# Kernel tuning notes

Measured on AMD Instinct MI355X. Metric: run time of the kernel, lower is better.

Reference implementation:

```python
import jax, jax.numpy as jnp
import numpy as np

NEG_INF = -jnp.inf


def setup_inputs() -> dict:
    B, V = 128, 128000
    key = jax.random.key(0)
    k1, k2, k3, k4, k5 = jax.random.split(key, 5)
    logits = jax.random.normal(k1, (B, V), dtype=jnp.float32)
    # temperatures in [0.1, 1.0) to avoid divide-by-tiny blowups
    temperatures = jax.random.uniform(k2, (B,), dtype=jnp.float32) * 0.9 + 0.1
    # min_p typically small, in [0, 0.1)
    min_ps = jax.random.uniform(k3, (B,), dtype=jnp.float32) * 0.1
    # top_p in [0.1, 1.0)
    top_ps = jax.random.uniform(k4, (B,), dtype=jnp.float32) * 0.9 + 0.1
    # top_k in [1, 1000)
    top_ks = jax.random.randint(k5, (B,), 1, 1000, dtype=jnp.int32)
    return {"logits": logits, "temperatures": temperatures, "min_ps": min_ps,
            "top_ps": top_ps, "top_ks": top_ks}


def _apply_top_k_top_p(logits, top_ps, top_ks):
    B, V = logits.shape
    sort_idx = jnp.argsort(logits, axis=-1)  # ascending, matches torch sort(descending=False)
    logits_sort = jnp.take_along_axis(logits, sort_idx, axis=-1)
    # top-k: threshold is the (V-k)-th smallest value; mask anything strictly below it
    thresh_idx = (V - top_ks.astype(jnp.int32))[:, None]          # [B,1]
    thresh = jnp.take_along_axis(logits_sort, thresh_idx, axis=-1)  # [B,1]
    logits_sort = jnp.where(logits_sort < thresh, NEG_INF, logits_sort)
    # top-p: drop smallest tokens whose cumulative prob <= 1 - p; never drop the max token
    probs_sort = jax.nn.softmax(logits_sort, axis=-1)
    probs_sum = jnp.cumsum(probs_sort, axis=-1)
    top_p_mask = probs_sum <= (1.0 - top_ps)[:, None]
    top_p_mask = top_p_mask.at[:, -1].set(False)
    logits_sort = jnp.where(top_p_mask, NEG_INF, logits_sort)
    # scatter back to original vocab order
    rows = jnp.arange(B)[:, None]
    return jnp.zeros_like(logits_sort).at[rows, sort_idx].set(logits_sort)


def _apply_min_p(logits, min_ps):
    probs = jax.nn.softmax(logits, axis=-1)
    top_probs = jnp.max(probs, axis=-1, keepdims=True)
    remove = probs < min_ps[:, None] * top_probs
    return jnp.where(remove, NEG_INF, logits)


def reference(logits, temperatures, min_ps, top_ps, top_ks):
    logits = logits.astype(jnp.float32) / temperatures[:, None]
    logits = _apply_top_k_top_p(logits, top_ps, top_ks)
    logits = _apply_min_p(logits, min_ps)
    # torch.multinomial(softmax(logits), 1) == categorical sampling from logits
    sample_key = jax.random.key(42)
    next_tokens = jax.random.categorical(sample_key, logits, axis=-1)  # [B]
    return next_tokens
```

## Files before the change

kernel.cpp:

```cpp
#include <hip/hip_runtime.h>
#include <stdint.h>

#define HBINS 8192
#define HSHIFT 19
#define CAND 2048
#define STHREADS 1024

typedef unsigned int u32;
typedef unsigned long long u64;

__device__ __forceinline__ u32 f2s(float f) {
  u32 b = __float_as_uint(f);
  return b ^ ((b & 0x80000000u) ? 0xFFFFFFFFu : 0x80000000u);
}
__device__ __forceinline__ float s2f(u32 s) {
  u32 b = (s & 0x80000000u) ? (s ^ 0x80000000u) : ~s;
  return __uint_as_float(b);
}
__device__ __forceinline__ u32 rotl32(u32 x, int r) { return (x << r) | (x >> (32 - r)); }

__device__ __forceinline__ u64 shfl_xor_u64(u64 v, int mask) {
  int lo = __shfl_xor((int)(u32)v, mask, 64);
  int hi = __shfl_xor((int)(u32)(v >> 32), mask, 64);
  return ((u64)(u32)hi << 32) | (u32)lo;
}
__device__ __forceinline__ u64 shfl_down_u64(u64 v, int delta) {
  int lo = __shfl_down((int)(u32)v, delta, 64);
  int hi = __shfl_down((int)(u32)(v >> 32), delta, 64);
  return ((u64)(u32)hi << 32) | (u32)lo;
}

__device__ __forceinline__ u32 threefry_bits(u32 ctr) {
  const u32 ks0 = 0u, ks1 = 42u, ks2 = 0x1BD11BDAu ^ 0u ^ 42u;
  u32 x0 = ks0;
  u32 x1 = ctr + ks1;
#define TFR(r) { x0 += x1; x1 = rotl32(x1, (r)); x1 ^= x0; }
  TFR(13) TFR(15) TFR(26) TFR(6)   x0 += ks1; x1 += ks2 + 1u;
  TFR(17) TFR(29) TFR(16) TFR(24)  x0 += ks2; x1 += ks0 + 2u;
  TFR(13) TFR(15) TFR(26) TFR(6)   x0 += ks0; x1 += ks1 + 3u;
  TFR(17) TFR(29) TFR(16) TFR(24)  x0 += ks1; x1 += ks2 + 4u;
  TFR(13) TFR(15) TFR(26) TFR(6)   x0 += ks2; x1 += ks0 + 5u;
#undef TFR
  return x0 ^ x1;
}

__global__ __launch_bounds__(STHREADS)
void Sampler_73529840107542_kernel(const float* __restrict__ logits,
                                   const float* __restrict__ temps,
                                   const float* __restrict__ minps,
                                   const float* __restrict__ topps,
                                   const int* __restrict__ topks,
                                   int* __restrict__ out, int V) {
  const int row = blockIdx.x;
  const int tid = threadIdx.x;
  const int w = tid >> 6;
  const int l = tid & 63;

  __shared__ __align__(16) unsigned char arena[69632];
  u32* hp     = (u32*)arena;
  u32* part   = (u32*)(arena + 65536);
  u64* cand   = (u64*)arena;
  u64* cand2  = (u64*)(arena + 16384);
  float* bufA = (float*)(arena + 16384);
  float* bufB = (float*)(arena + 24576);
  unsigned char* keepf = arena + 32768;
  float* redA = (float*)(arena + 16384);
  float* redB = (float*)(arena + 24576);

  __shared__ int sh_pstar, sh_cnt, sh_lb, sh_cs;
  __shared__ u32 sh_thr, sh_Ts;
  __shared__ float sh_m, sh_Z1, sh_Z2;
  __shared__ u32 wsum[16], wsuf[16];
  __shared__ u64 wbest[16];

  for (int i = tid; i < 2 * HBINS; i += STHREADS) hp[i] = 0u;
  __syncthreads();
  const float* src = logits + (size_t)row * (size_t)V;
  const u32 pc = (u32)(tid & 1);
  const int n4 = V >> 2;
  const float4* p4 = (const float4*)src;
  const int BB = STHREADS * 8;
  for (int base_i = 0; base_i < n4; base_i += BB) {
    float4 v[8];
    bool ok[8];
#pragma unroll
    for (int j = 0; j < 8; ++j) {
      int i = base_i + j * STHREADS + tid;
      ok[j] = (i < n4);
      v[j] = ok[j] ? p4[i] : float4{0.f, 0.f, 0.f, 0.f};
    }
#pragma unroll
    for (int j = 0; j < 8; ++j) {
      if (ok[j]) {
        atomicAdd(&hp[((f2s(v[j].x) >> HSHIFT) << 1) | pc], 1u);
        atomicAdd(&hp[((f2s(v[j].y) >> HSHIFT) << 1) | pc], 1u);
        atomicAdd(&hp[((f2s(v[j].z) >> HSHIFT) << 1) | pc], 1u);
        atomicAdd(&hp[((f2s(v[j].w) >> HSHIFT) << 1) | pc], 1u);
      }
    }
  }
  for (int i = (n4 << 2) + tid; i < V; i += STHREADS)
    atomicAdd(&hp[((f2s(src[i]) >> HSHIFT) << 1) | pc], 1u);
  __syncthreads();

  u32 pv;
  {
    u32 s = 0;
#pragma unroll
    for (int j = 0; j < 16; ++j) s += hp[tid * 16 + j];
    pv = s;
  }
#pragma unroll
  for (int d = 1; d < 64; d <<= 1) {
    u32 o = (u32)__shfl_down((int)pv, d, 64);
    if (l + d < 64) pv += o;
  }
  if (l == 0) wsum[w] = pv;
  __syncthreads();
  if (w == 0) {
    u32 v = (l < 16) ? wsum[l] : 0u;
#pragma unroll
    for (int d = 1; d < 64; d <<= 1) {
      u32 o = (u32)__shfl_down((int)v, d, 64);
      if (l + d < 64) v += o;
    }
    if (l < 16) wsuf[l] = v;
  }
  __syncthreads();
  part[tid] = pv + ((w < 15) ? wsuf[w + 1] : 0u);
  __syncthreads();

  int k = topks[row];
  if (k < 1) k = 1;
  if (k > V) k = V;
  const u32 ku = (u32)k;
  if (part[tid] >= ku && (tid == STHREADS - 1 || part[tid + 1] < ku))
    sh_pstar = tid;
  __syncthreads();
  {
    const int pstar = sh_pstar;
    const u32 tail = (pstar < STHREADS - 1) ? part[pstar + 1] : 0u;
    if (tid < 8) {
      u32 sb = tail;
      for (int j = 7; j >= tid; --j) sb += hp[(pstar * 8 + j) * 2] + hp[(pstar * 8 + j) * 2 + 1];
      u32 own = hp[(pstar * 8 + tid) * 2] + hp[(pstar * 8 + tid) * 2 + 1];
      if (sb >= ku && (tid == 7 || sb - own < ku)) {
        sh_thr = (u32)(pstar * 8 + tid) << HSHIFT;
        sh_cs = (int)((sb < (u32)CAND) ? sb : (u32)CAND);
      }
    }
    if (tid == 0) sh_cnt = 0;
  }
  __syncthreads();

  const u32 thr = sh_thr;
  const float t = temps[row];
  for (int base_i = 0; base_i < n4; base_i += BB) {
    float4 v[8];
    bool ok[8];
#pragma unroll
    for (int j = 0; j < 8; ++j) {
      int i = base_i + j * STHREADS + tid;
      ok[j] = (i < n4);
      v[j] = ok[j] ? p4[i] : float4{0.f, 0.f, 0.f, 0.f};
    }
#pragma unroll
    for (int j = 0; j < 8; ++j) {
      const int i = base_i + j * STHREADS + tid;
      float vals[4] = {v[j].x, v[j].y, v[j].z, v[j].w};
#pragma unroll
      for (int cmp = 0; cmp < 4; ++cmp) {
        bool pred = ok[j] && (f2s(vals[cmp]) >= thr);
        u64 mk = __ballot(pred);
        if (mk) {
          int leader = __ffsll((long long)mk) - 1;
          int tot = __popcll(mk);
          int b0 = 0;
          if (l == leader) b0 = atomicAdd(&sh_cnt, tot);
          b0 = __shfl(b0, leader, 64);
          if (pred) {
            int pos = b0 + __popcll(mk & ((1ull << l) - 1ull));
            if (pos < CAND)
              cand[pos] = ((u64)f2s(vals[cmp] / t) << 32) | (u32)(4 * i + cmp);
          }
        }
      }
    }
  }
  for (int i = (n4 << 2) + tid; i < V; i += STHREADS) {
    float x = src[i];
    if (f2s(x) >= thr) { int pos = atomicAdd(&sh_cnt, 1); if (pos < CAND) cand[pos] = ((u64)f2s(x / t) << 32) | (u32)i; }
  }
  __syncthreads();
  const int cs = sh_cs;

  const float one_minus_p = 1.0f - topps[row];
  const float minp = minps[row];
  const int e_lo = (w << 7) + l;
  const int e_hi = e_lo + 64;
  const u64 SENT = 0xFFFFFFFFFFFFFFFFull;
  u64 k0 = (e_lo < cs) ? cand[e_lo] : SENT;
  u64 k1 = (e_hi < cs) ? cand[e_hi] : SENT;
  __syncthreads();

  int P = 64;
  while (P < cs) P <<= 1;
  int pb = 0;
  for (int size = 2; size <= P; size <<= 1) {
    for (int s = size >> 1; s > 0; s >>= 1) {
      if (s >= 128) {
        u64* B = pb ? cand2 : cand;
        B[e_lo] = k0; B[e_hi] = k1;
        __syncthreads();
        u64 p0 = B[e_lo ^ s], p1 = B[e_hi ^ s];
        {
          bool keepmin = (((e_lo & s) == 0) == ((e_lo & size) == 0));
          if (keepmin ? (p0 < k0) : (p0 > k0)) k0 = p0;
        }
        {
          bool keepmin = (((e_hi & s) == 0) == ((e_hi & size) == 0));
          if (keepmin ? (p1 < k1) : (p1 > k1)) k1 = p1;
        }
        pb ^= 1;
      } else if (s == 64) {
        bool asc = ((e_lo & size) == 0);
        if ((k0 > k1) == asc) { u64 tt = k0; k0 = k1; k1 = tt; }
      } else {
        u64 p0 = shfl_xor_u64(k0, s);
        u64 p1 = shfl_xor_u64(k1, s);
        {
          bool keepmin = (((l & s) == 0) == ((e_lo & size) == 0));
          if (keepmin ? (p0 < k0) : (p0 > k0)) k0 = p0;
        }
        {
          bool keepmin = (((l & s) == 0) == ((e_hi & size) == 0));
          if (keepmin ? (p1 < k1) : (p1 > k1)) k1 = p1;
        }
      }
    }
  }
  __syncthreads();
  cand[e_lo] = k0; cand[e_hi] = k1;
  __syncthreads();

  if (tid == 0) {
    int ti = cs - k; if (ti < 0) ti = 0;
    sh_Ts = (u32)(cand[ti] >> 32);
    sh_m  = s2f((u32)(cand[cs - 1] >> 32));
  }
  __syncthreads();
  const u32 Ts = sh_Ts;
  const float m = sh_m;

  for (int c = tid; c < cs; c += STHREADS) {
    u32 s = (u32)(cand[c] >> 32);
    if (s >= Ts && (c == 0 || (u32)(cand[c - 1] >> 32) < Ts)) sh_lb = c;
  }
  __syncthreads();
  const int lb = sh_lb;

  {
    float e0 = 0.0f, e1 = 0.0f;
    const int c0 = tid, c1 = tid + STHREADS;
    if (c0 < cs) {
      u32 s = (u32)(cand[c0] >> 32);
      if (s >= Ts) e0 = expf(s2f(s) - m);
    }
    if (c1 < cs) {
      u32 s = (u32)(cand[c1] >> 32);
      if (s >= Ts) e1 = expf(s2f(s) - m);
    }
    bufA[c0] = e0;
    bufA[c1] = e1;
    redB[tid] = e0 + e1;
  }
  __syncthreads();
  for (int s = STHREADS >> 1; s >= 64; s >>= 1) {
    if (tid < s) redB[tid] += redB[tid + s];
    __syncthreads();
  }
  if (w == 0) {
    float v = redB[l];
    v += __shfl_down(v, 32, 64);
    v += __shfl_down(v, 16, 64);
    v += __shfl_down(v, 8, 64);
    v += __shfl_down(v, 4, 64);
    v += __shfl_down(v, 2, 64);
    v += __shfl_down(v, 1, 64);
    if (l == 0) sh_Z1 = v;
  }
  __syncthreads();
  const float Z1 = sh_Z1;

  if (w == 0) {
    float carry = 0.0f;
    for (int base = lb; base < cs; base += 64) {
      int c = base + l;
      float v = (c < cs) ? bufA[c] / Z1 : 0.0f;
      u32 vb = __float_as_uint(v);
      float acc = carry;
#pragma unroll
      for (int j = 0; j < 64; ++j) {
        float tt = __uint_as_float(__builtin_amdgcn_readlane(vb, j));
        acc += (l >= j) ? tt : 0.0f;
      }
      if (c < cs) bufB[c] = acc;
      carry = __uint_as_float(__builtin_amdgcn_readlane(__float_as_uint(acc), 63));
    }
  }
  __syncthreads();

  {
    float local = 0.0f;
    for (int c = tid; c < CAND; c += STHREADS) {
      unsigned char kf = 0;
      if (c < cs) {
        u32 s = (u32)(cand[c] >> 32);
        if (s >= Ts && (c == cs - 1 || bufB[c] > one_minus_p)) kf = 1;
        if (kf) local += expf(s2f(s) - m);
      }
      keepf[c] = kf;
    }
    redA[tid] = local;
  }
  __syncthreads();
  for (int s = STHREADS >> 1; s >= 64; s >>= 1) {
    if (tid < s) redA[tid] += redA[tid + s];
    __syncthreads();
  }
  if (w == 0) {
    float v = redA[l];
    v += __shfl_down(v, 32, 64);
    v += __shfl_down(v, 16, 64);
    v += __shfl_down(v, 8, 64);
    v += __shfl_down(v, 4, 64);
    v += __shfl_down(v, 2, 64);
    v += __shfl_down(v, 1, 64);
    if (l == 0) sh_Z2 = v;
  }
  __syncthreads();

  {
    const float Z2 = sh_Z2;
    const float rhs = minp * (1.0f / Z2);
    for (int c = tid; c < CAND; c += STHREADS) {
      if (keepf[c]) {
        u32 s = (u32)(cand[c] >> 32);
        float p2 = expf(s2f(s) - m) / Z2;
        if (p2 < rhs) keepf[c] = 0;
      }
    }
  }
  __syncthreads();

  {
    const float TINY = 1.17549435082228750797e-38f;
    u64 best = 0ull;
    for (int c = lb + tid; c < cs; c += STHREADS) {
      if (!keepf[c]) continue;
      u32 s = (u32)(cand[c] >> 32);
      u32 idx = (u32)(cand[c] & 0xFFFFFFFFull);
      float x = s2f(s);
      u32 bits = threefry_bits((u32)row * (u32)V + idx);
      float f = __uint_as_float((bits >> 9) | 0x3f800000u) - 1.0f;
      float u = fmaxf(TINY, f * 1.0f + TINY);
      float g = -logf(-logf(u));
      float sc = g + x;
      u64 key = ((u64)f2s(sc) << 32) | (u64)(0xFFFFFFFFu - idx);
      if (key > best) best = key;
    }
#pragma unroll
    for (int d = 32; d >= 1; d >>= 1) {
      u64 o = shfl_down_u64(best, d);
      if (o > best) best = o;
    }
    if (l == 0) wbest[w] = best;
    __syncthreads();
    if (w == 0) {
      u64 v = (l < 16) ? wbest[l] : 0ull;
#pragma unroll
      for (int d = 8; d >= 1; d >>= 1) {
        u64 o = shfl_down_u64(v, d);
        if (o > v) v = o;
      }
      if (l == 0) out[row] = (int)(0xFFFFFFFFu - (u32)(v & 0xFFFFFFFFull));
    }
  }
}

extern "C" void kernel_launch(void* const* d_in, const int* in_sizes, int n_in,
                              void* d_out, int out_size, void* d_ws, size_t ws_size,
                              hipStream_t stream) {
  const float* logits = (const float*)d_in[0];
  const float* temps  = (const float*)d_in[1];
  const float* minps  = (const float*)d_in[2];
  const float* topps  = (const float*)d_in[3];
  const int*   topks  = (const int*)d_in[4];
  const int B = in_sizes[1];
  const int V = in_sizes[0] / B;
  (void)n_in; (void)out_size; (void)d_ws; (void)ws_size;

  Sampler_73529840107542_kernel<<<dim3(B), dim3(STHREADS), 0, stream>>>(
      logits, temps, minps, topps, topks, (int*)d_out, V);
}
```

Before: 167.2 us.

## Stage high-logit candidates in LDS during histogram pass to skip second global scan

Result: slower. 189.7 us (+13.4%).

```diff
diff --git a/kernel.cpp b/kernel.cpp
--- a/kernel.cpp
+++ b/kernel.cpp
@@ -5,6 +5,7 @@
 #define HSHIFT 19
 #define CAND 2048
 #define STHREADS 1024
+#define STAGE_CAP 5120
 
 typedef unsigned int u32;
 typedef unsigned long long u64;
@@ -56,9 +57,10 @@
   const int w = tid >> 6;
   const int l = tid & 63;
 
-  __shared__ __align__(16) unsigned char arena[69632];
+  __shared__ __align__(16) unsigned char arena[110592];
   u32* hp     = (u32*)arena;
   u32* part   = (u32*)(arena + 65536);
+  u64* stage  = (u64*)(arena + 69632);
   u64* cand   = (u64*)arena;
   u64* cand2  = (u64*)(arena + 16384);
   float* bufA = (float*)(arena + 16384);
@@ -67,13 +69,17 @@
   float* redA = (float*)(arena + 16384);
   float* redB = (float*)(arena + 24576);
 
-  __shared__ int sh_pstar, sh_cnt, sh_lb, sh_cs;
+  __shared__ int sh_pstar, sh_cnt, sh_stg, sh_lb, sh_cs;
   __shared__ u32 sh_thr, sh_Ts;
   __shared__ float sh_m, sh_Z1, sh_Z2;
   __shared__ u32 wsum[16], wsuf[16];
   __shared__ u64 wbest[16];
 
+  const u32 SBIN = ((f2s(1.8f) >> HSHIFT) & ~7u);
+  const u32 sthr = SBIN << HSHIFT;
+
   for (int i = tid; i < 2 * HBINS; i += STHREADS) hp[i] = 0u;
+  if (tid == 0) sh_stg = 0;
   __syncthreads();
   const float* src = logits + (size_t)row * (size_t)V;
   const u32 pc = (u32)(tid & 1);
@@ -91,16 +97,41 @@
     }
 #pragma unroll
     for (int j = 0; j < 8; ++j) {
+      const int i = base_i + j * STHREADS + tid;
+      u32 fs[4] = {f2s(v[j].x), f2s(v[j].y), f2s(v[j].z), f2s(v[j].w)};
       if (ok[j]) {
-        atomicAdd(&hp[((f2s(v[j].x) >> HSHIFT) << 1) | pc], 1u);
-        atomicAdd(&hp[((f2s(v[j].y) >> HSHIFT) << 1) | pc], 1u);
-        atomicAdd(&hp[((f2s(v[j].z) >> HSHIFT) << 1) | pc], 1u);
-        atomicAdd(&hp[((f2s(v[j].w) >> HSHIFT) << 1) | pc], 1u);
-      }
-    }
-  }
-  for (int i = (n4 << 2) + tid; i < V; i += STHREADS)
-    atomicAdd(&hp[((f2s(src[i]) >> HSHIFT) << 1) | pc], 1u);
+        atomicAdd(&hp[((fs[0] >> HSHIFT) << 1) | pc], 1u);
+        atomicAdd(&hp[((fs[1] >> HSHIFT) << 1) | pc], 1u);
+        atomicAdd(&hp[((fs[2] >> HSHIFT) << 1) | pc], 1u);
+        atomicAdd(&hp[((fs[3] >> HSHIFT) << 1) | pc], 1u);
+      }
+#pragma unroll
+      for (int cmp = 0; cmp < 4; ++cmp) {
+        bool pred = ok[j] && (fs[cmp] >= sthr);
+        u64 mk = __ballot(pred);
+        if (mk) {
+          int leader = __ffsll((long long)mk) - 1;
+          int tot = __popcll(mk);
+          int b0 = 0;
+          if (l == leader) b0 = atomicAdd(&sh_stg, tot);
+          b0 = __shfl(b0, leader, 64);
+          if (pred) {
+            int pos = b0 + __popcll(mk & ((1ull << l) - 1ull));
+            if (pos < STAGE_CAP)
+              stage[pos] = ((u64)fs[cmp] << 32) | (u32)(4 * i + cmp);
+          }
+        }
+      }
+    }
+  }
+  for (int i = (n4 << 2) + tid; i < V; i += STHREADS) {
+    u32 fs = f2s(src[i]);
+    atomicAdd(&hp[((fs >> HSHIFT) << 1) | pc], 1u);
+    if (fs >= sthr) {
+      int pos = atomicAdd(&sh_stg, 1);
+      if (pos < STAGE_CAP) stage[pos] = ((u64)fs << 32) | (u32)i;
+    }
+  }
   __syncthreads();
 
   u32 pv;
@@ -155,41 +186,66 @@
 
   const u32 thr = sh_thr;
   const float t = temps[row];
-  for (int base_i = 0; base_i < n4; base_i += BB) {
-    float4 v[8];
-    bool ok[8];
-#pragma unroll
-    for (int j = 0; j < 8; ++j) {
-      int i = base_i + j * STHREADS + tid;
-      ok[j] = (i < n4);
-      v[j] = ok[j] ? p4[i] : float4{0.f, 0.f, 0.f, 0.f};
-    }
-#pragma unroll
-    for (int j = 0; j < 8; ++j) {
-      const int i = base_i + j * STHREADS + tid;
-      float vals[4] = {v[j].x, v[j].y, v[j].z, v[j].w};
-#pragma unroll
-      for (int cmp = 0; cmp < 4; ++cmp) {
-        bool pred = ok[j] && (f2s(vals[cmp]) >= thr);
-        u64 mk = __ballot(pred);
-        if (mk) {
-          int leader = __ffsll((long long)mk) - 1;
-          int tot = __popcll(mk);
-          int b0 = 0;
-          if (l == leader) b0 = atomicAdd(&sh_cnt, tot);
-          b0 = __shfl(b0, leader, 64);
-          if (pred) {
-            int pos = b0 + __popcll(mk & ((1ull << l) - 1ull));
-            if (pos < CAND)
-              cand[pos] = ((u64)f2s(vals[cmp] / t) << 32) | (u32)(4 * i + cmp);
+  const u32 staged_total = part[SBIN >> 3];
+  if (thr >= sthr && staged_total <= (u32)STAGE_CAP) {
+    const int sn = (int)staged_total;
+    for (int i0 = tid; i0 < sn; i0 += STHREADS) {
+      u64 e = stage[i0];
+      u32 hi = (u32)(e >> 32);
+      bool pred = (hi >= thr);
+      u64 mk = __ballot(pred);
+      if (mk) {
+        int leader = __ffsll((long long)mk) - 1;
+        int tot = __popcll(mk);
+        int b0 = 0;
+        if (l == leader) b0 = atomicAdd(&sh_cnt, tot);
+        b0 = __shfl(b0, leader, 64);
+        if (pred) {
+          int pos = b0 + __popcll(mk & ((1ull << l) - 1ull));
+          if (pos < CAND) {
+            float x = s2f(hi);
+            cand[pos] = ((u64)f2s(x / t) << 32) | (u32)(e & 0xFFFFFFFFull);
           }
         }
       }
     }
-  }
-  for (int i = (n4 << 2) + tid; i < V; i += STHREADS) {
-    float x = src[i];
-    if (f2s(x) >= thr) { int pos = atomicAdd(&sh_cnt, 1); if (pos < CAND) cand[pos] = ((u64)f2s(x / t) << 32) | (u32)i; }
+  } else {
+    for (int base_i = 0; base_i < n4; base_i += BB) {
+      float4 v[8];
+      bool ok[8];
+#pragma unroll
+      for (int j = 0; j < 8; ++j) {
+        int i = base_i + j * STHREADS + tid;
+        ok[j] = (i < n4);
+        v[j] = ok[j] ? p4[i] : float4{0.f, 0.f, 0.f, 0.f};
+      }
+#pragma unroll
+      for (int j = 0; j < 8; ++j) {
+        const int i = base_i + j * STHREADS + tid;
+        float vals[4] = {v[j].x, v[j].y, v[j].z, v[j].w};
+#pragma unroll
+        for (int cmp = 0; cmp < 4; ++cmp) {
+          bool pred = ok[j] && (f2s(vals[cmp]) >= thr);
+          u64 mk = __ballot(pred);
+          if (mk) {
+            int leader = __ffsll((long long)mk) - 1;
+            int tot = __popcll(mk);
+            int b0 = 0;
+            if (l == leader) b0 = atomicAdd(&sh_cnt, tot);
+            b0 = __shfl(b0, leader, 64);
+            if (pred) {
+              int pos = b0 + __popcll(mk & ((1ull << l) - 1ull));
+              if (pos < CAND)
+                cand[pos] = ((u64)f2s(vals[cmp] / t) << 32) | (u32)(4 * i + cmp);
+            }
+          }
+        }
+      }
+    }
+    for (int i = (n4 << 2) + tid; i < V; i += STHREADS) {
+      float x = src[i];
+      if (f2s(x) >= thr) { int pos = atomicAdd(&sh_cnt, 1); if (pos < CAND) cand[pos] = ((u64)f2s(x / t) << 32) | (u32)i; }
+    }
   }
   __syncthreads();
   const int cs = sh_cs;
```
